# Kernel optimization log

Measured on AMD Instinct MI355X. Metric: run time of the kernel, lower is better.

Reference implementation:

```python
import jax, jax.numpy as jnp
import numpy as np

NUM_HEADS = 16
HEAD_DIM = 64
ROPE_BASE = 10000.0


def _rope_cos_sin(seq_len, head_dim, dtype):
    inv_freq = 1.0 / (ROPE_BASE ** (jnp.arange(0, head_dim, 2, dtype=jnp.float32) / head_dim))
    t = jnp.arange(seq_len, dtype=jnp.float32)
    freqs = t[:, None] * inv_freq[None, :]          # (S, head_dim/2)
    emb = jnp.concatenate([freqs, freqs], axis=-1)  # (S, head_dim)
    return jnp.cos(emb).astype(dtype), jnp.sin(emb).astype(dtype)


def _rotate_half(x):
    x1, x2 = jnp.split(x, 2, axis=-1)
    return jnp.concatenate([-x2, x1], axis=-1)


def setup_inputs() -> dict:
    key = jax.random.key(0)
    k1, k2, k3 = jax.random.split(key, 3)
    B, S, D = 2, 2048, 1024
    x = jax.random.normal(k1, (B, S, D), dtype=jnp.float32)
    Wq = jax.random.normal(k2, (D, D), dtype=jnp.float32) * (D ** -0.5)
    Wkv = jax.random.normal(k3, (2 * D, D), dtype=jnp.float32) * (D ** -0.5)
    mask = jnp.tril(jnp.ones((S, S), dtype=jnp.int32))  # causal mask
    return {"x": x, "Wq": Wq, "Wkv": Wkv, "mask": mask}


def reference(x, Wq, Wkv, mask):
    B, S, D = x.shape
    H, Hd = NUM_HEADS, HEAD_DIM

    # projections (torch Linear: x @ W.T)
    q = (x @ Wq.T).reshape(B, S, H, Hd).transpose(0, 2, 1, 3)           # (B,H,S,Hd)
    kv = (x @ Wkv.T).reshape(B, S, H, Hd, 2).transpose(0, 2, 1, 3, 4)   # (B,H,S,Hd,2)
    k = kv[..., 0]
    v = kv[..., 1]

    # RoPE
    cos, sin = _rope_cos_sin(S, Hd, x.dtype)  # (S,Hd) broadcast over (B,H)
    q = q * cos + _rotate_half(q) * sin
    k = k * cos + _rotate_half(k) * sin

    # attention with full score materialization (faithful to source)
    scale = 1.0 / jnp.sqrt(jnp.asarray(Hd, dtype=x.dtype))
    scores = jnp.einsum('bhqd,bhkd->bhqk', q, k) * scale                # (B,H,S,S)
    scores = jnp.where(mask == 0, -jnp.inf, scores)
    attn = jax.nn.softmax(scores, axis=-1)
    out = jnp.einsum('bhqk,bhkd->bhqd', attn, v)                        # (B,H,S,Hd)
    return out.transpose(0, 2, 1, 3).reshape(B, S, D)
```

## Files before the change

kernel.cpp:

```cpp
#include <hip/hip_runtime.h>
#include <hip/hip_bf16.h>
#include <math.h>


typedef short bfrag __attribute__((ext_vector_type(8)));
typedef float f32x4 __attribute__((ext_vector_type(4)));

__device__ __forceinline__ float bf2f(ushort u) {
    union { uint i; float f; } v; v.i = ((uint)u) << 16; return v.f;
}
__device__ __forceinline__ ushort f2bf(float f) {
    union { uint i; float f; } v; v.f = f;
    uint u = v.i;
    return (ushort)((u + 0x7fffu + ((u >> 16) & 1u)) >> 16);
}

#define MFMA16 __builtin_amdgcn_mfma_f32_16x16x32_bf16

__device__ __forceinline__ void gl_lds16(const ushort* g, ushort* l) {
    __builtin_amdgcn_global_load_lds(
        (const __attribute__((address_space(1))) void*)g,
        (__attribute__((address_space(3))) void*)l, 16, 0, 0);
}

__global__ __launch_bounds__(256)
void cvt_bf16(const float* __restrict__ x, const float* __restrict__ wq,
              const float* __restrict__ wkv, ushort* __restrict__ xb,
              ushort* __restrict__ wb)
{
    const size_t NX = 4096u * 1024u, NWQ = 1024u * 1024u;
    size_t i8 = ((size_t)blockIdx.x * 256 + threadIdx.x) * 8;
    const float* src;
    ushort* dst;
    if (i8 < NX) { src = x + i8; dst = xb + i8; }
    else {
        size_t j = i8 - NX;
        dst = wb + j;
        src = (j < NWQ) ? (wq + j) : (wkv + (j - NWQ));
    }
    float4 a = *(const float4*)(src);
    float4 c = *(const float4*)(src + 4);
    ushort u[8];
    u[0] = f2bf(a.x); u[1] = f2bf(a.y); u[2] = f2bf(a.z); u[3] = f2bf(a.w);
    u[4] = f2bf(c.x); u[5] = f2bf(c.y); u[6] = f2bf(c.z); u[7] = f2bf(c.w);
    *(uint4*)dst = *(uint4*)u;
}

__global__ __launch_bounds__(256)
void rope_table(float2* __restrict__ tab)
{
    int t  = blockIdx.x * 256 + threadIdx.x;
    int fi = t & 31, s = t >> 5;
    float invf = (float)exp((double)fi * -0.28782313662425574);
    float thf  = (float)s * invf;
    const double TWO_PI = 6.283185307179586476925287;
    double th = (double)thf;
    double kq = __builtin_rint(th * (1.0 / TWO_PI));
    float r = (float)(th - kq * TWO_PI);
    tab[t] = make_float2(cosf(r), sinf(r));
}

__global__ __launch_bounds__(256)
void gemm_qkv(const ushort* __restrict__ xb, const ushort* __restrict__ wb,
              const float2* __restrict__ tab, ushort* __restrict__ Qb,
              ushort* __restrict__ Kb, ushort* __restrict__ Vt)
{
    __shared__ ushort Ash[128][32];
    __shared__ ushort Bsh[128][32];

    const int tid  = threadIdx.x;
    const int lane = tid & 63, wv = tid >> 6;
    const int quad = lane >> 4, li = lane & 15;
    const int m0 = blockIdx.x * 128, n0 = blockIdx.y * 128;

    f32x4 acc[2][8];
#pragma unroll
    for (int mi = 0; mi < 2; mi++)
#pragma unroll
        for (int j = 0; j < 8; j++) acc[mi][j] = (f32x4){0.f, 0.f, 0.f, 0.f};

    const int rsub = lane >> 2, kofs = (lane & 3) * 8;
    const ushort* gA0 = xb + (size_t)(m0 + wv * 32 + rsub) * 1024 + kofs;
    const ushort* gA1 = gA0 + 16 * 1024;
    const ushort* gB0 = wb + (size_t)(n0 + wv * 32 + rsub) * 1024 + kofs;
    const ushort* gB1 = gB0 + 16 * 1024;

    for (int k0 = 0; k0 < 1024; k0 += 32) {
        __syncthreads();
        gl_lds16(gA0 + k0, &Ash[wv * 32][0]);
        gl_lds16(gA1 + k0, &Ash[wv * 32 + 16][0]);
        gl_lds16(gB0 + k0, &Bsh[wv * 32][0]);
        gl_lds16(gB1 + k0, &Bsh[wv * 32 + 16][0]);
        __syncthreads();

        bfrag af[2], bf[8];
#pragma unroll
        for (int mi = 0; mi < 2; mi++)
            af[mi] = *(const bfrag*)&Ash[wv * 32 + mi * 16 + li][quad * 8];
#pragma unroll
        for (int j = 0; j < 8; j++)
            bf[j] = *(const bfrag*)&Bsh[j * 16 + li][quad * 8];
#pragma unroll
        for (int mi = 0; mi < 2; mi++)
#pragma unroll
            for (int j = 0; j < 8; j++)
                acc[mi][j] = MFMA16(af[mi], bf[j], acc[mi][j], 0, 0, 0);
    }

    if (n0 < 1024) {
        const int hbase = n0 >> 6;
#pragma unroll
        for (int mi = 0; mi < 2; mi++)
#pragma unroll
            for (int r = 0; r < 4; r++) {
                int m = m0 + wv * 32 + mi * 16 + quad * 4 + r;
                int bb = m >> 11, s = m & 2047;
                float2 t0 = tab[s * 32 + li];
                float2 t1 = tab[s * 32 + li + 16];
#pragma unroll
                for (int j = 0; j < 8; j++) {
                    float v  = acc[mi][j][r];
                    float vp = acc[mi][j ^ 2][r];
                    float2 tt = (j & 1) ? t1 : t0;
                    float rh = (j & 2) ? vp : -vp;
                    int h = hbase + (j >> 2), hd = (j & 3) * 16 + li;
                    Qb[(size_t)((bb * 16 + h) * 2048 + s) * 64 + hd] =
                        f2bf(v * tt.x + rh * tt.y);
                }
            }
    } else {
        const int h = (n0 - 1024) >> 7;
        const int li2 = li >> 1;
        if ((li & 1) == 0) {
#pragma unroll
            for (int mi = 0; mi < 2; mi++)
#pragma unroll
                for (int r = 0; r < 4; r++) {
                    int m = m0 + wv * 32 + mi * 16 + quad * 4 + r;
                    int bb = m >> 11, s = m & 2047;
                    float2 tt4[4];
#pragma unroll
                    for (int jj = 0; jj < 4; jj++)
                        tt4[jj] = tab[s * 32 + jj * 8 + li2];
#pragma unroll
                    for (int j = 0; j < 8; j++) {
                        float v  = acc[mi][j][r];
                        float vp = acc[mi][j ^ 4][r];
                        float2 tt = tt4[j & 3];
                        float rh = (j & 4) ? vp : -vp;
                        int hd = j * 8 + li2;
                        Kb[(size_t)((bb * 16 + h) * 2048 + s) * 64 + hd] =
                            f2bf(v * tt.x + rh * tt.y);
                    }
                }
        } else {
#pragma unroll
            for (int mi = 0; mi < 2; mi++) {
                int m4 = m0 + wv * 32 + mi * 16 + quad * 4;
                int bb = m4 >> 11, s0 = m4 & 2047;
#pragma unroll
                for (int j = 0; j < 8; j++) {
                    int hd = j * 8 + li2;
                    ushort u4[4];
#pragma unroll
                    for (int r = 0; r < 4; r++) u4[r] = f2bf(acc[mi][j][r]);
                    *(ushort4*)&Vt[(size_t)((bb * 16 + h) * 64 + hd) * 2048 + s0] =
                        *(ushort4*)u4;
                }
            }
        }
    }
}

__global__ __launch_bounds__(256)
void attn(const ushort* __restrict__ Qb, const ushort* __restrict__ Kb,
          const ushort* __restrict__ Vt, float* __restrict__ out)
{
    __shared__ ushort Ksh[64][72];
    __shared__ ushort Vsh[64][72];
    __shared__ ushort Psh[8][16][80];

    const int tid  = threadIdx.x;
    const int lane = tid & 63, w = tid >> 6;
    const int quad = lane >> 4, li = lane & 15;

    const int l  = (int)blockIdx.y * 16 + (int)blockIdx.x;
    const int bh = l & 31;
    const int i  = l >> 5;
    const int t  = (i < 8) ? i : 23 - i;
    const int qtS = t, qtB = 31 - t;
    const int b = bh >> 4, h = bh & 15;

    const int rowB = qtB * 64 + w * 16 + li;
    const int rowS = qtS * 64 + w * 16 + li;
    const ushort* qpB = Qb + (size_t)(bh * 2048 + rowB) * 64;
    const ushort* qpS = Qb + (size_t)(bh * 2048 + rowS) * 64;
    bfrag qaB0 = *(const bfrag*)(qpB + quad * 8);
    bfrag qaB1 = *(const bfrag*)(qpB + quad * 8 + 32);
    bfrag qaS0 = *(const bfrag*)(qpS + quad * 8);
    bfrag qaS1 = *(const bfrag*)(qpS + quad * 8 + 32);

    f32x4 oB[4], oS[4];
#pragma unroll
    for (int j = 0; j < 4; j++) {
        oB[j] = (f32x4){0.f, 0.f, 0.f, 0.f};
        oS[j] = (f32x4){0.f, 0.f, 0.f, 0.f};
    }
    float lrowB = 0.f, lrowS = 0.f;

    const int srow = tid >> 2, sc0 = (tid & 3) * 16;
    const ushort* kbase = Kb + (size_t)bh * 2048 * 64;
    const ushort* vbase = Vt + (size_t)bh * 64 * 2048;

    uint4 ka, kb_, va, vb_;
    {
        const ushort* gk = kbase + (size_t)srow * 64 + sc0;
        ka  = *(const uint4*)gk;
        kb_ = *(const uint4*)(gk + 8);
        const ushort* gv = vbase + (size_t)srow * 2048 + sc0;
        va  = *(const uint4*)gv;
        vb_ = *(const uint4*)(gv + 8);
    }

    const float C = 0.125f * 1.4426950408889634f;

    for (int kt = 0; kt <= qtB; ++kt) {
        __syncthreads();
        *(uint4*)&Ksh[srow][sc0]     = ka;
        *(uint4*)&Ksh[srow][sc0 + 8] = kb_;
        *(uint4*)&Vsh[srow][sc0]     = va;
        *(uint4*)&Vsh[srow][sc0 + 8] = vb_;
        __syncthreads();

        if (kt < qtB) {
            const ushort* gk = kbase + (size_t)((kt + 1) * 64 + srow) * 64 + sc0;
            ka  = *(const uint4*)gk;
            kb_ = *(const uint4*)(gk + 8);
            const ushort* gv = vbase + (size_t)srow * 2048 + (kt + 1) * 64 + sc0;
            va  = *(const uint4*)gv;
            vb_ = *(const uint4*)(gv + 8);
        }

        const bool doS = (kt <= qtS);
        float rsB = 0.f, rsS = 0.f;

#pragma unroll
        for (int j = 0; j < 4; j++) {
            bfrag kf0 = *(const bfrag*)&Ksh[j * 16 + li][quad * 8];
            bfrag kf1 = *(const bfrag*)&Ksh[j * 16 + li][quad * 8 + 32];

            __builtin_amdgcn_s_setprio(1);
            f32x4 zB = (f32x4){0.f, 0.f, 0.f, 0.f};
            zB = MFMA16(kf0, qaB0, zB, 0, 0, 0);
            zB = MFMA16(kf1, qaB1, zB, 0, 0, 0);
            f32x4 zS = (f32x4){0.f, 0.f, 0.f, 0.f};
            if (doS) {
                zS = MFMA16(kf0, qaS0, zS, 0, 0, 0);
                zS = MFMA16(kf1, qaS1, zS, 0, 0, 0);
            }
            __builtin_amdgcn_s_setprio(0);

            if (kt == qtB) {
                int kg0 = kt * 64 + j * 16 + quad * 4;
#pragma unroll
                for (int r = 0; r < 4; r++)
                    zB[r] = (kg0 + r <= rowB) ? zB[r] : -3.0e38f;
            }
            if (doS && kt == qtS) {
                int kg0 = kt * 64 + j * 16 + quad * 4;
#pragma unroll
                for (int r = 0; r < 4; r++)
                    zS[r] = (kg0 + r <= rowS) ? zS[r] : -3.0e38f;
            }

            ushort pkB[4];
#pragma unroll
            for (int r = 0; r < 4; r++) {
                float pv = exp2f(zB[r] * C);
                uint pu = __float_as_uint(pv);
                pkB[r] = (ushort)(pu >> 16);
                rsB += __uint_as_float(pu & 0xffff0000u);
            }
            *(ushort4*)&Psh[w * 2][li][j * 16 + quad * 4] = *(ushort4*)pkB;

            if (doS) {
                ushort pkS[4];
#pragma unroll
                for (int r = 0; r < 4; r++) {
                    float pv = exp2f(zS[r] * C);
                    uint pu = __float_as_uint(pv);
                    pkS[r] = (ushort)(pu >> 16);
                    rsS += __uint_as_float(pu & 0xffff0000u);
                }
                *(ushort4*)&Psh[w * 2 + 1][li][j * 16 + quad * 4] = *(ushort4*)pkS;
            }
        }

        rsB += __shfl_xor(rsB, 16);
        rsB += __shfl_xor(rsB, 32);
        lrowB += rsB;
        if (doS) {
            rsS += __shfl_xor(rsS, 16);
            rsS += __shfl_xor(rsS, 32);
            lrowS += rsS;
        }

        asm volatile("s_waitcnt lgkmcnt(0)" ::: "memory");
        bfrag paB0 = *(const bfrag*)&Psh[w * 2][li][quad * 8];
        bfrag paB1 = *(const bfrag*)&Psh[w * 2][li][quad * 8 + 32];
        bfrag paS0, paS1;
        if (doS) {
            paS0 = *(const bfrag*)&Psh[w * 2 + 1][li][quad * 8];
            paS1 = *(const bfrag*)&Psh[w * 2 + 1][li][quad * 8 + 32];
        }

#pragma unroll
        for (int j = 0; j < 4; j++) {
            bfrag vf0 = *(const bfrag*)&Vsh[j * 16 + li][quad * 8];
            bfrag vf1 = *(const bfrag*)&Vsh[j * 16 + li][quad * 8 + 32];
            __builtin_amdgcn_s_setprio(1);
            oB[j] = MFMA16(paB0, vf0, oB[j], 0, 0, 0);
            oB[j] = MFMA16(paB1, vf1, oB[j], 0, 0, 0);
            if (doS) {
                oS[j] = MFMA16(paS0, vf0, oS[j], 0, 0, 0);
                oS[j] = MFMA16(paS1, vf1, oS[j], 0, 0, 0);
            }
            __builtin_amdgcn_s_setprio(0);
        }
    }

    float lfB[4], lfS[4];
#pragma unroll
    for (int r = 0; r < 4; r++) {
        lfB[r] = __shfl(lrowB, (lane & 48) + quad * 4 + r);
        lfS[r] = __shfl(lrowS, (lane & 48) + quad * 4 + r);
    }

#pragma unroll
    for (int j = 0; j < 4; j++)
#pragma unroll
        for (int r = 0; r < 4; r++) {
            int sB = qtB * 64 + w * 16 + quad * 4 + r;
            out[(size_t)(b * 2048 + sB) * 1024 + h * 64 + j * 16 + li] =
                oB[j][r] / lfB[r];
            int sS = qtS * 64 + w * 16 + quad * 4 + r;
            out[(size_t)(b * 2048 + sS) * 1024 + h * 64 + j * 16 + li] =
                oS[j][r] / lfS[r];
        }
}

extern "C" void kernel_launch(void* const* d_in, const int* in_sizes, int n_in,
                              void* d_out, int out_size, void* d_ws, size_t ws_size,
                              hipStream_t stream)
{
    (void)in_sizes; (void)n_in; (void)out_size; (void)ws_size;
    const float* x   = (const float*)d_in[0];
    const float* wq  = (const float*)d_in[1];
    const float* wkv = (const float*)d_in[2];

    ushort* xb = (ushort*)d_ws;
    ushort* wb = xb + (size_t)4096 * 1024;
    float2* tab = (float2*)(wb + (size_t)3072 * 1024);
    ushort* Qb = (ushort*)(tab + 65536);
    ushort* Kb = Qb + (size_t)2 * 16 * 2048 * 64;
    ushort* Vt = Kb + (size_t)2 * 16 * 2048 * 64;
    float* out = (float*)d_out;

    cvt_bf16<<<3584, 256, 0, stream>>>(x, wq, wkv, xb, wb);
    rope_table<<<256, 256, 0, stream>>>(tab);
    dim3 g1(32, 24);
    gemm_qkv<<<g1, 256, 0, stream>>>(xb, wb, tab, Qb, Kb, Vt);
    dim3 g4(16, 32);
    attn<<<g4, 256, 0, stream>>>(Qb, Kb, Vt, out);
}
```

Measured before the change: 186.6 us.

## Widen GEMM K-tile with swizzled LDS, double-buffer attention K/V, use hardware bf16 rounding

The QKV GEMM now stages 64-wide K slices per iteration. It uses an XOR-swizzled LDS layout to avoid bank conflicts and halves the number of barrier pairs per K sweep. The attention kernel double-buffers K/V tiles in LDS so that one barrier per iteration replaces two, and the next tile's store overlaps compute. The softmax probabilities now use round-to-nearest bf16 conversion with an unrounded fp32 row sum instead of truncation. This adds LDS usage and slightly more conversion work.

```diff
diff --git a/kernel.cpp b/kernel.cpp
--- a/kernel.cpp
+++ b/kernel.cpp
@@ -13,6 +13,11 @@
     union { uint i; float f; } v; v.f = f;
     uint u = v.i;
     return (ushort)((u + 0x7fffu + ((u >> 16) & 1u)) >> 16);
+}
+__device__ __forceinline__ ushort f2bf_hw(float f) {
+    union { __hip_bfloat16 b; ushort u; } cv;
+    cv.b = __float2bfloat16(f);
+    return cv.u;
 }
 
 #define MFMA16 __builtin_amdgcn_mfma_f32_16x16x32_bf16
@@ -65,8 +70,8 @@
               const float2* __restrict__ tab, ushort* __restrict__ Qb,
               ushort* __restrict__ Kb, ushort* __restrict__ Vt)
 {
-    __shared__ ushort Ash[128][32];
-    __shared__ ushort Bsh[128][32];
+    __shared__ ushort Ash[128][64];
+    __shared__ ushort Bsh[128][64];
 
     const int tid  = threadIdx.x;
     const int lane = tid & 63, wv = tid >> 6;
@@ -79,32 +84,38 @@
 #pragma unroll
         for (int j = 0; j < 8; j++) acc[mi][j] = (f32x4){0.f, 0.f, 0.f, 0.f};
 
-    const int rsub = lane >> 2, kofs = (lane & 3) * 8;
-    const ushort* gA0 = xb + (size_t)(m0 + wv * 32 + rsub) * 1024 + kofs;
-    const ushort* gA1 = gA0 + 16 * 1024;
-    const ushort* gB0 = wb + (size_t)(n0 + wv * 32 + rsub) * 1024 + kofs;
-    const ushort* gB1 = gB0 + 16 * 1024;
-
-    for (int k0 = 0; k0 < 1024; k0 += 32) {
+    const int r8  = lane >> 3;
+    const int gch = ((lane & 7) ^ r8) * 8;
+    const ushort* gA = xb + (size_t)(m0 + wv * 32 + r8) * 1024 + gch;
+    const ushort* gB = wb + (size_t)(n0 + wv * 32 + r8) * 1024 + gch;
+
+    for (int k0 = 0; k0 < 1024; k0 += 64) {
         __syncthreads();
-        gl_lds16(gA0 + k0, &Ash[wv * 32][0]);
-        gl_lds16(gA1 + k0, &Ash[wv * 32 + 16][0]);
-        gl_lds16(gB0 + k0, &Bsh[wv * 32][0]);
-        gl_lds16(gB1 + k0, &Bsh[wv * 32 + 16][0]);
+#pragma unroll
+        for (int c = 0; c < 4; c++) {
+            gl_lds16(gA + (size_t)(c * 8) * 1024 + k0, &Ash[wv * 32 + c * 8][0]);
+            gl_lds16(gB + (size_t)(c * 8) * 1024 + k0, &Bsh[wv * 32 + c * 8][0]);
+        }
         __syncthreads();
 
-        bfrag af[2], bf[8];
-#pragma unroll
-        for (int mi = 0; mi < 2; mi++)
-            af[mi] = *(const bfrag*)&Ash[wv * 32 + mi * 16 + li][quad * 8];
-#pragma unroll
-        for (int j = 0; j < 8; j++)
-            bf[j] = *(const bfrag*)&Bsh[j * 16 + li][quad * 8];
-#pragma unroll
-        for (int mi = 0; mi < 2; mi++)
+        const int sw = li & 7;
+#pragma unroll
+        for (int ks = 0; ks < 2; ks++) {
+            bfrag af[2], bf[8];
+#pragma unroll
+            for (int mi = 0; mi < 2; mi++)
+                af[mi] = *(const bfrag*)
+                    &Ash[wv * 32 + mi * 16 + li][(((ks << 2) | quad) ^ sw) * 8];
 #pragma unroll
             for (int j = 0; j < 8; j++)
-                acc[mi][j] = MFMA16(af[mi], bf[j], acc[mi][j], 0, 0, 0);
+                bf[j] = *(const bfrag*)
+                    &Bsh[j * 16 + li][(((ks << 2) | quad) ^ sw) * 8];
+#pragma unroll
+            for (int mi = 0; mi < 2; mi++)
+#pragma unroll
+                for (int j = 0; j < 8; j++)
+                    acc[mi][j] = MFMA16(af[mi], bf[j], acc[mi][j], 0, 0, 0);
+        }
     }
 
     if (n0 < 1024) {
@@ -176,9 +187,9 @@
 void attn(const ushort* __restrict__ Qb, const ushort* __restrict__ Kb,
           const ushort* __restrict__ Vt, float* __restrict__ out)
 {
-    __shared__ ushort Ksh[64][72];
-    __shared__ ushort Vsh[64][72];
-    __shared__ ushort Psh[8][16][80];
+    __shared__ ushort Ksh[2][64][72];
+    __shared__ ushort Vsh[2][64][72];
+    __shared__ ushort Psh[8][16][72];
 
     const int tid  = threadIdx.x;
     const int lane = tid & 63, w = tid >> 6;
@@ -215,30 +226,44 @@
     uint4 ka, kb_, va, vb_;
     {
         const ushort* gk = kbase + (size_t)srow * 64 + sc0;
+        uint4 t0 = *(const uint4*)gk;
+        uint4 t1 = *(const uint4*)(gk + 8);
+        const ushort* gv = vbase + (size_t)srow * 2048 + sc0;
+        uint4 t2 = *(const uint4*)gv;
+        uint4 t3 = *(const uint4*)(gv + 8);
+        *(uint4*)&Ksh[0][srow][sc0]     = t0;
+        *(uint4*)&Ksh[0][srow][sc0 + 8] = t1;
+        *(uint4*)&Vsh[0][srow][sc0]     = t2;
+        *(uint4*)&Vsh[0][srow][sc0 + 8] = t3;
+    }
+    {
+        const ushort* gk = kbase + (size_t)(64 + srow) * 64 + sc0;
         ka  = *(const uint4*)gk;
         kb_ = *(const uint4*)(gk + 8);
-        const ushort* gv = vbase + (size_t)srow * 2048 + sc0;
+        const ushort* gv = vbase + (size_t)srow * 2048 + 64 + sc0;
         va  = *(const uint4*)gv;
         vb_ = *(const uint4*)(gv + 8);
     }
+    __syncthreads();
 
     const float C = 0.125f * 1.4426950408889634f;
 
     for (int kt = 0; kt <= qtB; ++kt) {
-        __syncthreads();
-        *(uint4*)&Ksh[srow][sc0]     = ka;
-        *(uint4*)&Ksh[srow][sc0 + 8] = kb_;
-        *(uint4*)&Vsh[srow][sc0]     = va;
-        *(uint4*)&Vsh[srow][sc0 + 8] = vb_;
-        __syncthreads();
+        const int cur = kt & 1;
 
         if (kt < qtB) {
-            const ushort* gk = kbase + (size_t)((kt + 1) * 64 + srow) * 64 + sc0;
-            ka  = *(const uint4*)gk;
-            kb_ = *(const uint4*)(gk + 8);
-            const ushort* gv = vbase + (size_t)srow * 2048 + (kt + 1) * 64 + sc0;
-            va  = *(const uint4*)gv;
-            vb_ = *(const uint4*)(gv + 8);
+            *(uint4*)&Ksh[cur ^ 1][srow][sc0]     = ka;
+            *(uint4*)&Ksh[cur ^ 1][srow][sc0 + 8] = kb_;
+            *(uint4*)&Vsh[cur ^ 1][srow][sc0]     = va;
+            *(uint4*)&Vsh[cur ^ 1][srow][sc0 + 8] = vb_;
+            if (kt + 1 < qtB) {
+                const ushort* gk = kbase + (size_t)((kt + 2) * 64 + srow) * 64 + sc0;
+                ka  = *(const uint4*)gk;
+                kb_ = *(const uint4*)(gk + 8);
+                const ushort* gv = vbase + (size_t)srow * 2048 + (kt + 2) * 64 + sc0;
+                va  = *(const uint4*)gv;
+                vb_ = *(const uint4*)(gv + 8);
+            }
         }
 
         const bool doS = (kt <= qtS);
@@ -246,8 +271,8 @@
 
 #pragma unroll
         for (int j = 0; j < 4; j++) {
-            bfrag kf0 = *(const bfrag*)&Ksh[j * 16 + li][quad * 8];
-            bfrag kf1 = *(const bfrag*)&Ksh[j * 16 + li][quad * 8 + 32];
+            bfrag kf0 = *(const bfrag*)&Ksh[cur][j * 16 + li][quad * 8];
+            bfrag kf1 = *(const bfrag*)&Ksh[cur][j * 16 + li][quad * 8 + 32];
 
             __builtin_amdgcn_s_setprio(1);
             f32x4 zB = (f32x4){0.f, 0.f, 0.f, 0.f};
@@ -277,9 +302,8 @@
 #pragma unroll
             for (int r = 0; r < 4; r++) {
                 float pv = exp2f(zB[r] * C);
-                uint pu = __float_as_uint(pv);
-                pkB[r] = (ushort)(pu >> 16);
-                rsB += __uint_as_float(pu & 0xffff0000u);
+                rsB += pv;
+                pkB[r] = f2bf_hw(pv);
             }
             *(ushort4*)&Psh[w * 2][li][j * 16 + quad * 4] = *(ushort4*)pkB;
 
@@ -288,9 +312,8 @@
 #pragma unroll
                 for (int r = 0; r < 4; r++) {
                     float pv = exp2f(zS[r] * C);
-                    uint pu = __float_as_uint(pv);
-                    pkS[r] = (ushort)(pu >> 16);
-                    rsS += __uint_as_float(pu & 0xffff0000u);
+                    rsS += pv;
+                    pkS[r] = f2bf_hw(pv);
                 }
                 *(ushort4*)&Psh[w * 2 + 1][li][j * 16 + quad * 4] = *(ushort4*)pkS;
             }
@@ -316,8 +339,8 @@
 
 #pragma unroll
         for (int j = 0; j < 4; j++) {
-            bfrag vf0 = *(const bfrag*)&Vsh[j * 16 + li][quad * 8];
-            bfrag vf1 = *(const bfrag*)&Vsh[j * 16 + li][quad * 8 + 32];
+            bfrag vf0 = *(const bfrag*)&Vsh[cur][j * 16 + li][quad * 8];
+            bfrag vf1 = *(const bfrag*)&Vsh[cur][j * 16 + li][quad * 8 + 32];
             __builtin_amdgcn_s_setprio(1);
             oB[j] = MFMA16(paB0, vf0, oB[j], 0, 0, 0);
             oB[j] = MFMA16(paB1, vf1, oB[j], 0, 0, 0);
@@ -327,6 +350,8 @@
             }
             __builtin_amdgcn_s_setprio(0);
         }
+
+        __syncthreads();
     }
 
     float lfB[4], lfS[4];
```

Result: faster. 181.2 us (-2.9%).
